# Performance work log

Measured on AMD Instinct MI355X. Metric: run time of the kernel, lower is better.

## Reference

```python
import jax, jax.numpy as jnp
import numpy as np

B, S, D = 32, 8192, 256  # batch, src_len, dim (context features = 2*D)


def setup_inputs() -> dict:
    key = jax.random.key(0)
    k0, k1, k2, k3, k4, k5 = jax.random.split(key, 6)
    inp = jax.random.normal(k0, (B, 1, D), jnp.float32)
    context = jax.random.normal(k1, (B, S, 2 * D), jnp.float32)
    Wa = jax.random.normal(k2, (D, D), jnp.float32) / np.sqrt(D)      # torch Linear weight [out,in]
    Ua = jax.random.normal(k3, (D, 2 * D), jnp.float32) / np.sqrt(2 * D)
    va = jax.random.normal(k4, (1, D), jnp.float32) / np.sqrt(D)
    context_lengths = jax.random.randint(k5, (B,), S // 2, S + 1).astype(jnp.int32)
    return {"input": inp, "context": context, "Wa": Wa, "Ua": Ua,
            "va": va, "context_lengths": context_lengths}


def reference(input, context, Wa, Ua, va, context_lengths):
    # score: va(Wa(h_t) + Ua(h_s)) -- additive (Bahdanau) attention, no nonlinearity
    q = jnp.einsum('btd,ed->bte', input, Wa)            # [B,1,D]
    k = jnp.einsum('bsc,ec->bse', context, Ua)          # [B,S,D]
    align = jnp.einsum('bsd,d->bs', q + k, va[0])       # [B,S] (targetL=1, squeezed)
    # mask positions >= context_lengths with -inf (sequence_mask + masked_fill_)
    mask = jnp.arange(S, dtype=jnp.int32)[None, :] < context_lengths[:, None]
    align = jnp.where(mask, align, -jnp.inf)
    attn = jax.nn.softmax(align, axis=-1)               # [B,S]
    c = jnp.einsum('bs,bsc->bc', attn, context)         # [B,2D]  (bmm)
    # 3D input with targetL=1 -> non-one-step branch: transpose(0,1)
    attn_h = c[None]                                    # [1,B,2D]
    align_vectors = attn[None]                          # [1,B,S]
    return attn_h, align_vectors
```

## Files before the change

### kernel.cpp

```cpp
#include <hip/hip_runtime.h>
#include <math.h>

#define Bn 32
#define Sn 8192
#define Dn 256
#define Cn 512
#define NBLK 1024
#define NEG_BIG (-1e30f)

#define WS_U     0
#define WS_QV    512
#define WS_PM    544
#define WS_PL    (WS_PM + NBLK)
#define WS_PLAN  (WS_PL + NBLK)
#define WS_ALIGN (WS_PLAN + NBLK)
#define WS_PACC  (WS_ALIGN + Bn * Sn)

__device__ inline void ga_partition(const int* __restrict__ lens, int k,
                                    int& b, int& t0, int& t1) {
  int TOT = 0;
#pragma unroll
  for (int i = 0; i < Bn; ++i) TOT += (lens[i] + 15) >> 4;
  int P = 0, bb = 0, offb = 0, cntb = 1, ntb = 1;
#pragma unroll
  for (int i = 0; i < Bn; ++i) {
    const int nt = (lens[i] + 15) >> 4;
    const int o0 = (P * NBLK) / TOT;
    const int o1 = ((P + nt) * NBLK) / TOT;
    if (k >= o0 && k < o1) { bb = i; offb = o0; cntb = o1 - o0; ntb = nt; }
    P += nt;
  }
  const int j = k - offb;
  b = bb;
  t0 = (j * ntb) / cntb;
  t1 = ((j + 1) * ntb) / cntb;
}

__device__ inline void ga_batch_range(const int* __restrict__ lens, int b,
                                      int& offb, int& cntb) {
  int TOT = 0;
#pragma unroll
  for (int i = 0; i < Bn; ++i) TOT += (lens[i] + 15) >> 4;
  int P = 0;
  for (int i = 0; i < b; ++i) P += (lens[i] + 15) >> 4;
  const int nt = (lens[b] + 15) >> 4;
  offb = (P * NBLK) / TOT;
  cntb = ((P + nt) * NBLK) / TOT - offb;
}

__global__ __launch_bounds__(256) void ga_prep(const float* __restrict__ input,
                                               const float* __restrict__ Wa,
                                               const float* __restrict__ Ua,
                                               const float* __restrict__ va,
                                               const int* __restrict__ lens,
                                               float* __restrict__ ws) {
  const int tid = threadIdx.x, bx = blockIdx.x;
  if (bx < 8) {
    const int c = bx * 64 + (tid & 63);
    const int q = tid >> 6;
    float acc = 0.f;
#pragma unroll 8
    for (int i = 0; i < 64; ++i) {
      const int d = q * 64 + i;
      acc += va[d] * Ua[(size_t)d * Cn + c];
    }
    __shared__ float sh[4][64];
    sh[q][tid & 63] = acc;
    __syncthreads();
    if (tid < 64)
      ws[WS_U + bx * 64 + tid] = sh[0][tid] + sh[1][tid] + sh[2][tid] + sh[3][tid];
  } else if (bx == 8) {
    __shared__ float wsh[Dn];
    float acc = 0.f;
#pragma unroll 8
    for (int e = 0; e < Dn; ++e)
      acc += va[e] * Wa[(size_t)e * Dn + tid];
    wsh[tid] = acc;
    __syncthreads();
    const int b = tid >> 3, l8 = tid & 7;
    float p = 0.f;
#pragma unroll
    for (int j = 0; j < Dn / 8; ++j) {
      const int d = l8 + j * 8;
      p += input[b * Dn + d] * wsh[d];
    }
    p += __shfl_xor(p, 1);
    p += __shfl_xor(p, 2);
    p += __shfl_xor(p, 4);
    if (l8 == 0) ws[WS_QV + b] = p;
  } else {
    const int k = (bx - 9) * 256 + tid;
    int b, t0, t1;
    ga_partition(lens, k, b, t0, t1);
    ((int*)ws)[WS_PLAN + k] = b | (t0 << 5) | (t1 << 17);
  }
}

__global__ __launch_bounds__(256, 4) void ga_main(const float* __restrict__ context,
                                                  const int* __restrict__ lens,
                                                  float* __restrict__ ws) {
  const int k = blockIdx.x;
  const int plan = ((const int*)ws)[WS_PLAN + k];
  const int b  = plan & 31;
  const int t0 = (plan >> 5)  & 0xFFF;
  const int t1 = (plan >> 17) & 0xFFF;
  const int tid  = threadIdx.x;
  const int wave = tid >> 6;
  const int lane = tid & 63;
  const int l16  = lane & 15;
  const int slot = lane >> 4;
  const int len = lens[b];
  const float qv = ws[WS_QV + b];

  const float4* uv = (const float4*)(ws + WS_U);
  float4 u0 = uv[l16 +  0], u1 = uv[l16 + 16], u2 = uv[l16 + 32], u3 = uv[l16 + 48];
  float4 u4 = uv[l16 + 64], u5 = uv[l16 + 80], u6 = uv[l16 + 96], u7 = uv[l16 + 112];

  float m = NEG_BIG, l = 0.f;
  float4 a0 = make_float4(0.f,0.f,0.f,0.f), a1 = a0, a2 = a0, a3 = a0;
  float4 a4 = a0, a5 = a0, a6 = a0, a7 = a0;

  const float* cbase = context + (size_t)b * Sn * Cn;
  float* alout = ws + WS_ALIGN + (size_t)b * Sn;

  for (int t = t0; t < t1; ++t) {
    const int s = t * 16 + wave * 4 + slot;
    const float4* p = (const float4*)(cbase + (size_t)s * Cn) + l16;
    const float4 f0 = p[0],  f1 = p[16], f2 = p[32], f3 = p[48];
    const float4 f4 = p[64], f5 = p[80], f6 = p[96], f7 = p[112];

    float dot = f0.x*u0.x + f0.y*u0.y + f0.z*u0.z + f0.w*u0.w
              + f1.x*u1.x + f1.y*u1.y + f1.z*u1.z + f1.w*u1.w
              + f2.x*u2.x + f2.y*u2.y + f2.z*u2.z + f2.w*u2.w
              + f3.x*u3.x + f3.y*u3.y + f3.z*u3.z + f3.w*u3.w
              + f4.x*u4.x + f4.y*u4.y + f4.z*u4.z + f4.w*u4.w
              + f5.x*u5.x + f5.y*u5.y + f5.z*u5.z + f5.w*u5.w
              + f6.x*u6.x + f6.y*u6.y + f6.z*u6.z + f6.w*u6.w
              + f7.x*u7.x + f7.y*u7.y + f7.z*u7.z + f7.w*u7.w;
    dot += __shfl_xor(dot, 1);
    dot += __shfl_xor(dot, 2);
    dot += __shfl_xor(dot, 4);
    dot += __shfl_xor(dot, 8);

    const bool valid = (s < len);
    const float al = valid ? (qv + dot) : -INFINITY;
    if (l16 == 0 && valid) alout[s] = al;

    const float mn = fmaxf(m, al);
    const float sc = __expf(m - mn);
    const float pw = __expf(al - mn);
    l = l * sc + pw;
    a0.x=a0.x*sc+pw*f0.x; a0.y=a0.y*sc+pw*f0.y; a0.z=a0.z*sc+pw*f0.z; a0.w=a0.w*sc+pw*f0.w;
    a1.x=a1.x*sc+pw*f1.x; a1.y=a1.y*sc+pw*f1.y; a1.z=a1.z*sc+pw*f1.z; a1.w=a1.w*sc+pw*f1.w;
    a2.x=a2.x*sc+pw*f2.x; a2.y=a2.y*sc+pw*f2.y; a2.z=a2.z*sc+pw*f2.z; a2.w=a2.w*sc+pw*f2.w;
    a3.x=a3.x*sc+pw*f3.x; a3.y=a3.y*sc+pw*f3.y; a3.z=a3.z*sc+pw*f3.z; a3.w=a3.w*sc+pw*f3.w;
    a4.x=a4.x*sc+pw*f4.x; a4.y=a4.y*sc+pw*f4.y; a4.z=a4.z*sc+pw*f4.z; a4.w=a4.w*sc+pw*f4.w;
    a5.x=a5.x*sc+pw*f5.x; a5.y=a5.y*sc+pw*f5.y; a5.z=a5.z*sc+pw*f5.z; a5.w=a5.w*sc+pw*f5.w;
    a6.x=a6.x*sc+pw*f6.x; a6.y=a6.y*sc+pw*f6.y; a6.z=a6.z*sc+pw*f6.z; a6.w=a6.w*sc+pw*f6.w;
    a7.x=a7.x*sc+pw*f7.x; a7.y=a7.y*sc+pw*f7.y; a7.z=a7.z*sc+pw*f7.z; a7.w=a7.w*sc+pw*f7.w;
    m = mn;
  }

  float mw = fmaxf(m, __shfl_xor(m, 16));
  mw = fmaxf(mw, __shfl_xor(mw, 32));
  const float fS = __expf(m - mw);
  float lw = l * fS;
  lw += __shfl_xor(lw, 16);
  lw += __shfl_xor(lw, 32);
#define MRG(A) \
  A.x*=fS; A.y*=fS; A.z*=fS; A.w*=fS; \
  A.x+=__shfl_xor(A.x,16); A.y+=__shfl_xor(A.y,16); A.z+=__shfl_xor(A.z,16); A.w+=__shfl_xor(A.w,16); \
  A.x+=__shfl_xor(A.x,32); A.y+=__shfl_xor(A.y,32); A.z+=__shfl_xor(A.z,32); A.w+=__shfl_xor(A.w,32);
  MRG(a0) MRG(a1) MRG(a2) MRG(a3) MRG(a4) MRG(a5) MRG(a6) MRG(a7)
#undef MRG

  __shared__ float msh[4], lsh[4];
  __shared__ float accsh[4][Cn];
  if (lane == 0) { msh[wave] = mw; lsh[wave] = lw; }
  if (slot == 0) {
    float4* arow = (float4*)accsh[wave];
    arow[l16 +  0] = a0;  arow[l16 + 16] = a1;
    arow[l16 + 32] = a2;  arow[l16 + 48] = a3;
    arow[l16 + 64] = a4;  arow[l16 + 80] = a5;
    arow[l16 + 96] = a6;  arow[l16 +112] = a7;
  }
  __syncthreads();

  const float M = fmaxf(fmaxf(msh[0], msh[1]), fmaxf(msh[2], msh[3]));
  const float e0 = __expf(msh[0] - M), e1 = __expf(msh[1] - M);
  const float e2 = __expf(msh[2] - M), e3 = __expf(msh[3] - M);
  float* pacc = ws + WS_PACC + (size_t)k * Cn;
  for (int ch = tid; ch < Cn; ch += 256)
    pacc[ch] = e0 * accsh[0][ch] + e1 * accsh[1][ch]
             + e2 * accsh[2][ch] + e3 * accsh[3][ch];
  if (tid == 0) {
    ws[WS_PM + k] = M;
    ws[WS_PL + k] = e0 * lsh[0] + e1 * lsh[1] + e2 * lsh[2] + e3 * lsh[3];
  }
}

__global__ __launch_bounds__(256) void ga_finalize(const float* __restrict__ ws,
                                                   const int* __restrict__ lens,
                                                   float* __restrict__ out) {
  const int b = blockIdx.x >> 3, p = blockIdx.x & 7;
  const int tid = threadIdx.x;
  int offb, cntb;
  ga_batch_range(lens, b, offb, cntb);

  __shared__ float wgt[128];
  __shared__ float red[4][64];
  __shared__ float Msh, Lish;

  if (tid < 64) {
    const float m0 = (tid      < cntb) ? ws[WS_PM + offb + tid]      : NEG_BIG;
    const float m1 = (tid + 64 < cntb) ? ws[WS_PM + offb + tid + 64] : NEG_BIG;
    float mm = fmaxf(m0, m1);
#pragma unroll
    for (int off = 32; off; off >>= 1) mm = fmaxf(mm, __shfl_xor(mm, off));
    const float w0 = __expf(m0 - mm);
    const float w1 = __expf(m1 - mm);
    wgt[tid] = w0;  wgt[tid + 64] = w1;
    float li = 0.f;
    if (tid      < cntb) li += ws[WS_PL + offb + tid]      * w0;
    if (tid + 64 < cntb) li += ws[WS_PL + offb + tid + 64] * w1;
#pragma unroll
    for (int off = 32; off; off >>= 1) li += __shfl_xor(li, off);
    if (tid == 0) { Msh = mm; Lish = 1.f / li; }
  }
  __syncthreads();
  const float M = Msh, Li = Lish;

  {
    const int c = p * 64 + (tid & 63), g = tid >> 6;
    const float* pacc = ws + WS_PACC + (size_t)offb * Cn;
    float s = 0.f;
    for (int i = g; i < cntb; i += 4) s += wgt[i] * pacc[(size_t)i * Cn + c];
    red[g][tid & 63] = s;
    __syncthreads();
    if (tid < 64)
      out[b * Cn + p * 64 + tid] =
          (red[0][tid] + red[1][tid] + red[2][tid] + red[3][tid]) * Li;
  }

  {
    const int len = lens[b];
    const float* al = ws + WS_ALIGN + (size_t)b * Sn;
    float* ao = out + Bn * Cn + (size_t)b * Sn;
    const int s0 = p * 1024 + tid * 4;
    const float4 v = *(const float4*)(al + s0);
    float4 o;
    o.x = (s0 + 0 < len) ? __expf(v.x - M) * Li : 0.f;
    o.y = (s0 + 1 < len) ? __expf(v.y - M) * Li : 0.f;
    o.z = (s0 + 2 < len) ? __expf(v.z - M) * Li : 0.f;
    o.w = (s0 + 3 < len) ? __expf(v.w - M) * Li : 0.f;
    *(float4*)(ao + s0) = o;
  }
}

extern "C" void kernel_launch(void* const* d_in, const int* in_sizes, int n_in,
                              void* d_out, int out_size, void* d_ws, size_t ws_size,
                              hipStream_t stream) {
  const float* input   = (const float*)d_in[0];
  const float* context = (const float*)d_in[1];
  const float* Wa      = (const float*)d_in[2];
  const float* Ua      = (const float*)d_in[3];
  const float* va      = (const float*)d_in[4];
  const int*   lens    = (const int*)d_in[5];
  float* out = (float*)d_out;
  float* ws  = (float*)d_ws;

  ga_prep<<<13, 256, 0, stream>>>(input, Wa, Ua, va, lens, ws);
  ga_main<<<NBLK, 256, 0, stream>>>(context, lens, ws);
  ga_finalize<<<Bn * 8, 256, 0, stream>>>(ws, lens, out);
}
```

Before: 102.7 us.

## Double-buffer context loads, shrink block count, and restructure prep/finalize reductions

The main loop is rewritten to prefetch the next 16-row tile of context into a second register set while the current tile is processed, aiming to hide global-memory latency. The block count drops from 1024 to 768 and the occupancy hint from 4 to 3 blocks per CU, making room for the extra registers. The u-vector prep now uses float4 loads with a 16-way reduction. Finalize now runs on 32 blocks per batch and reduces with wave shuffles instead of shared memory. The risks are register pressure from the doubled buffers and finalize assuming at most 64 partitions per batch.

```diff
diff --git a/kernel.cpp b/kernel.cpp
--- a/kernel.cpp
+++ b/kernel.cpp
@@ -5,7 +5,7 @@
 #define Sn 8192
 #define Dn 256
 #define Cn 512
-#define NBLK 1024
+#define NBLK 768
 #define NEG_BIG (-1e30f)
 
 #define WS_U     0
@@ -56,19 +56,27 @@
                                                float* __restrict__ ws) {
   const int tid = threadIdx.x, bx = blockIdx.x;
   if (bx < 8) {
-    const int c = bx * 64 + (tid & 63);
-    const int q = tid >> 6;
-    float acc = 0.f;
-#pragma unroll 8
-    for (int i = 0; i < 64; ++i) {
-      const int d = q * 64 + i;
-      acc += va[d] * Ua[(size_t)d * Cn + c];
-    }
-    __shared__ float sh[4][64];
-    sh[q][tid & 63] = acc;
+    const float4* Ua4 = (const float4*)Ua;
+    const int rg = tid >> 4, q = tid & 15;
+    float4 acc = make_float4(0.f, 0.f, 0.f, 0.f);
+#pragma unroll 4
+    for (int d = rg; d < Dn; d += 16) {
+      const float vd = va[d];
+      const float4 t = Ua4[(size_t)d * 128 + bx * 16 + q];
+      acc.x += vd * t.x; acc.y += vd * t.y; acc.z += vd * t.z; acc.w += vd * t.w;
+    }
+    __shared__ float4 sh4[16][16];
+    sh4[rg][q] = acc;
     __syncthreads();
-    if (tid < 64)
-      ws[WS_U + bx * 64 + tid] = sh[0][tid] + sh[1][tid] + sh[2][tid] + sh[3][tid];
+    if (tid < 16) {
+      float4 s = sh4[0][tid];
+#pragma unroll
+      for (int r = 1; r < 16; ++r) {
+        s.x += sh4[r][tid].x; s.y += sh4[r][tid].y;
+        s.z += sh4[r][tid].z; s.w += sh4[r][tid].w;
+      }
+      ((float4*)(ws + WS_U))[bx * 16 + tid] = s;
+    }
   } else if (bx == 8) {
     __shared__ float wsh[Dn];
     float acc = 0.f;
@@ -96,7 +104,46 @@
   }
 }
 
-__global__ __launch_bounds__(256, 4) void ga_main(const float* __restrict__ context,
+#define LOADT(F0,F1,F2,F3,F4,F5,F6,F7, T) do {                       \
+    const int s_ = (T) * 16 + wave * 4 + slot;                       \
+    const float4* p_ = (const float4*)(cbase + (size_t)s_ * Cn) + l16;\
+    F0 = p_[0];  F1 = p_[16]; F2 = p_[32]; F3 = p_[48];              \
+    F4 = p_[64]; F5 = p_[80]; F6 = p_[96]; F7 = p_[112];             \
+  } while (0)
+
+#define PROC(F0,F1,F2,F3,F4,F5,F6,F7, T) do {                        \
+    const int s_ = (T) * 16 + wave * 4 + slot;                       \
+    float dot = F0.x*u0.x + F0.y*u0.y + F0.z*u0.z + F0.w*u0.w        \
+              + F1.x*u1.x + F1.y*u1.y + F1.z*u1.z + F1.w*u1.w        \
+              + F2.x*u2.x + F2.y*u2.y + F2.z*u2.z + F2.w*u2.w        \
+              + F3.x*u3.x + F3.y*u3.y + F3.z*u3.z + F3.w*u3.w        \
+              + F4.x*u4.x + F4.y*u4.y + F4.z*u4.z + F4.w*u4.w        \
+              + F5.x*u5.x + F5.y*u5.y + F5.z*u5.z + F5.w*u5.w        \
+              + F6.x*u6.x + F6.y*u6.y + F6.z*u6.z + F6.w*u6.w        \
+              + F7.x*u7.x + F7.y*u7.y + F7.z*u7.z + F7.w*u7.w;       \
+    dot += __shfl_xor(dot, 1);                                       \
+    dot += __shfl_xor(dot, 2);                                       \
+    dot += __shfl_xor(dot, 4);                                       \
+    dot += __shfl_xor(dot, 8);                                       \
+    const bool valid = (s_ < len);                                   \
+    const float al = valid ? (qv + dot) : -INFINITY;                 \
+    if (l16 == 0 && valid) alout[s_] = al;                           \
+    const float mn = fmaxf(m, al);                                   \
+    const float sc = __expf(m - mn);                                 \
+    const float pw = __expf(al - mn);                                \
+    l = l * sc + pw;                                                 \
+    a0.x=a0.x*sc+pw*F0.x; a0.y=a0.y*sc+pw*F0.y; a0.z=a0.z*sc+pw*F0.z; a0.w=a0.w*sc+pw*F0.w; \
+    a1.x=a1.x*sc+pw*F1.x; a1.y=a1.y*sc+pw*F1.y; a1.z=a1.z*sc+pw*F1.z; a1.w=a1.w*sc+pw*F1.w; \
+    a2.x=a2.x*sc+pw*F2.x; a2.y=a2.y*sc+pw*F2.y; a2.z=a2.z*sc+pw*F2.z; a2.w=a2.w*sc+pw*F2.w; \
+    a3.x=a3.x*sc+pw*F3.x; a3.y=a3.y*sc+pw*F3.y; a3.z=a3.z*sc+pw*F3.z; a3.w=a3.w*sc+pw*F3.w; \
+    a4.x=a4.x*sc+pw*F4.x; a4.y=a4.y*sc+pw*F4.y; a4.z=a4.z*sc+pw*F4.z; a4.w=a4.w*sc+pw*F4.w; \
+    a5.x=a5.x*sc+pw*F5.x; a5.y=a5.y*sc+pw*F5.y; a5.z=a5.z*sc+pw*F5.z; a5.w=a5.w*sc+pw*F5.w; \
+    a6.x=a6.x*sc+pw*F6.x; a6.y=a6.y*sc+pw*F6.y; a6.z=a6.z*sc+pw*F6.z; a6.w=a6.w*sc+pw*F6.w; \
+    a7.x=a7.x*sc+pw*F7.x; a7.y=a7.y*sc+pw*F7.y; a7.z=a7.z*sc+pw*F7.z; a7.w=a7.w*sc+pw*F7.w; \
+    m = mn;                                                          \
+  } while (0)
+
+__global__ __launch_bounds__(256, 3) void ga_main(const float* __restrict__ context,
                                                   const int* __restrict__ lens,
                                                   float* __restrict__ ws) {
   const int k = blockIdx.x;
@@ -123,43 +170,21 @@
   const float* cbase = context + (size_t)b * Sn * Cn;
   float* alout = ws + WS_ALIGN + (size_t)b * Sn;
 
-  for (int t = t0; t < t1; ++t) {
-    const int s = t * 16 + wave * 4 + slot;
-    const float4* p = (const float4*)(cbase + (size_t)s * Cn) + l16;
-    const float4 f0 = p[0],  f1 = p[16], f2 = p[32], f3 = p[48];
-    const float4 f4 = p[64], f5 = p[80], f6 = p[96], f7 = p[112];
-
-    float dot = f0.x*u0.x + f0.y*u0.y + f0.z*u0.z + f0.w*u0.w
-              + f1.x*u1.x + f1.y*u1.y + f1.z*u1.z + f1.w*u1.w
-              + f2.x*u2.x + f2.y*u2.y + f2.z*u2.z + f2.w*u2.w
-              + f3.x*u3.x + f3.y*u3.y + f3.z*u3.z + f3.w*u3.w
-              + f4.x*u4.x + f4.y*u4.y + f4.z*u4.z + f4.w*u4.w
-              + f5.x*u5.x + f5.y*u5.y + f5.z*u5.z + f5.w*u5.w
-              + f6.x*u6.x + f6.y*u6.y + f6.z*u6.z + f6.w*u6.w
-              + f7.x*u7.x + f7.y*u7.y + f7.z*u7.z + f7.w*u7.w;
-    dot += __shfl_xor(dot, 1);
-    dot += __shfl_xor(dot, 2);
-    dot += __shfl_xor(dot, 4);
-    dot += __shfl_xor(dot, 8);
-
-    const bool valid = (s < len);
-    const float al = valid ? (qv + dot) : -INFINITY;
-    if (l16 == 0 && valid) alout[s] = al;
-
-    const float mn = fmaxf(m, al);
-    const float sc = __expf(m - mn);
-    const float pw = __expf(al - mn);
-    l = l * sc + pw;
-    a0.x=a0.x*sc+pw*f0.x; a0.y=a0.y*sc+pw*f0.y; a0.z=a0.z*sc+pw*f0.z; a0.w=a0.w*sc+pw*f0.w;
-    a1.x=a1.x*sc+pw*f1.x; a1.y=a1.y*sc+pw*f1.y; a1.z=a1.z*sc+pw*f1.z; a1.w=a1.w*sc+pw*f1.w;
-    a2.x=a2.x*sc+pw*f2.x; a2.y=a2.y*sc+pw*f2.y; a2.z=a2.z*sc+pw*f2.z; a2.w=a2.w*sc+pw*f2.w;
-    a3.x=a3.x*sc+pw*f3.x; a3.y=a3.y*sc+pw*f3.y; a3.z=a3.z*sc+pw*f3.z; a3.w=a3.w*sc+pw*f3.w;
-    a4.x=a4.x*sc+pw*f4.x; a4.y=a4.y*sc+pw*f4.y; a4.z=a4.z*sc+pw*f4.z; a4.w=a4.w*sc+pw*f4.w;
-    a5.x=a5.x*sc+pw*f5.x; a5.y=a5.y*sc+pw*f5.y; a5.z=a5.z*sc+pw*f5.z; a5.w=a5.w*sc+pw*f5.w;
-    a6.x=a6.x*sc+pw*f6.x; a6.y=a6.y*sc+pw*f6.y; a6.z=a6.z*sc+pw*f6.z; a6.w=a6.w*sc+pw*f6.w;
-    a7.x=a7.x*sc+pw*f7.x; a7.y=a7.y*sc+pw*f7.y; a7.z=a7.z*sc+pw*f7.z; a7.w=a7.w*sc+pw*f7.w;
-    m = mn;
-  }
+  float4 fa0, fa1, fa2, fa3, fa4, fa5, fa6, fa7;
+  float4 fb0, fb1, fb2, fb3, fb4, fb5, fb6, fb7;
+
+  int t = t0;
+  LOADT(fa0,fa1,fa2,fa3,fa4,fa5,fa6,fa7, t0);
+  while (t + 1 < t1) {
+    LOADT(fb0,fb1,fb2,fb3,fb4,fb5,fb6,fb7, t + 1);
+    PROC (fa0,fa1,fa2,fa3,fa4,fa5,fa6,fa7, t);
+    if (t + 2 < t1)
+      LOADT(fa0,fa1,fa2,fa3,fa4,fa5,fa6,fa7, t + 2);
+    PROC (fb0,fb1,fb2,fb3,fb4,fb5,fb6,fb7, t + 1);
+    t += 2;
+  }
+  if (t < t1)
+    PROC (fa0,fa1,fa2,fa3,fa4,fa5,fa6,fa7, t);
 
   float mw = fmaxf(m, __shfl_xor(m, 16));
   mw = fmaxf(mw, __shfl_xor(mw, 32));
@@ -202,58 +227,46 @@
 __global__ __launch_bounds__(256) void ga_finalize(const float* __restrict__ ws,
                                                    const int* __restrict__ lens,
                                                    float* __restrict__ out) {
-  const int b = blockIdx.x >> 3, p = blockIdx.x & 7;
+  const int b = blockIdx.x >> 5, p = blockIdx.x & 31;
   const int tid = threadIdx.x;
+  const int wave = tid >> 6, lane = tid & 63;
   int offb, cntb;
   ga_batch_range(lens, b, offb, cntb);
 
-  __shared__ float wgt[128];
-  __shared__ float red[4][64];
-  __shared__ float Msh, Lish;
-
-  if (tid < 64) {
-    const float m0 = (tid      < cntb) ? ws[WS_PM + offb + tid]      : NEG_BIG;
-    const float m1 = (tid + 64 < cntb) ? ws[WS_PM + offb + tid + 64] : NEG_BIG;
-    float mm = fmaxf(m0, m1);
-#pragma unroll
-    for (int off = 32; off; off >>= 1) mm = fmaxf(mm, __shfl_xor(mm, off));
-    const float w0 = __expf(m0 - mm);
-    const float w1 = __expf(m1 - mm);
-    wgt[tid] = w0;  wgt[tid + 64] = w1;
-    float li = 0.f;
-    if (tid      < cntb) li += ws[WS_PL + offb + tid]      * w0;
-    if (tid + 64 < cntb) li += ws[WS_PL + offb + tid + 64] * w1;
-#pragma unroll
-    for (int off = 32; off; off >>= 1) li += __shfl_xor(li, off);
-    if (tid == 0) { Msh = mm; Lish = 1.f / li; }
-  }
-  __syncthreads();
-  const float M = Msh, Li = Lish;
+  const float mi = (lane < cntb) ? ws[WS_PM + offb + lane] : NEG_BIG;
+  float mm = mi;
+#pragma unroll
+  for (int off = 32; off; off >>= 1) mm = fmaxf(mm, __shfl_xor(mm, off));
+  const float wgt = __expf(mi - mm);
+  float li = (lane < cntb) ? ws[WS_PL + offb + lane] * wgt : 0.f;
+#pragma unroll
+  for (int off = 32; off; off >>= 1) li += __shfl_xor(li, off);
+  const float Li = 1.f / li;
 
   {
-    const int c = p * 64 + (tid & 63), g = tid >> 6;
+    const int cc = lane >> 4, ii = lane & 15;
+    const int c = p * 16 + wave * 4 + cc;
     const float* pacc = ws + WS_PACC + (size_t)offb * Cn;
     float s = 0.f;
-    for (int i = g; i < cntb; i += 4) s += wgt[i] * pacc[(size_t)i * Cn + c];
-    red[g][tid & 63] = s;
-    __syncthreads();
-    if (tid < 64)
-      out[b * Cn + p * 64 + tid] =
-          (red[0][tid] + red[1][tid] + red[2][tid] + red[3][tid]) * Li;
+#pragma unroll
+    for (int kk = 0; kk < 4; ++kk) {
+      const int i = ii + 16 * kk;
+      const float w = __shfl(wgt, i);
+      if (i < cntb) s += w * pacc[(size_t)i * Cn + c];
+    }
+    s += __shfl_xor(s, 1);
+    s += __shfl_xor(s, 2);
+    s += __shfl_xor(s, 4);
+    s += __shfl_xor(s, 8);
+    if (ii == 0) out[b * Cn + c] = s * Li;
   }
 
   {
     const int len = lens[b];
+    const int s0 = p * 256 + tid;
     const float* al = ws + WS_ALIGN + (size_t)b * Sn;
-    float* ao = out + Bn * Cn + (size_t)b * Sn;
-    const int s0 = p * 1024 + tid * 4;
-    const float4 v = *(const float4*)(al + s0);
-    float4 o;
-    o.x = (s0 + 0 < len) ? __expf(v.x - M) * Li : 0.f;
-    o.y = (s0 + 1 < len) ? __expf(v.y - M) * Li : 0.f;
-    o.z = (s0 + 2 < len) ? __expf(v.z - M) * Li : 0.f;
-    o.w = (s0 + 3 < len) ? __expf(v.w - M) * Li : 0.f;
-    *(float4*)(ao + s0) = o;
+    out[Bn * Cn + (size_t)b * Sn + s0] =
+        (s0 < len) ? __expf(al[s0] - mm) * Li : 0.f;
   }
 }
 
@@ -269,7 +282,7 @@
   float* out = (float*)d_out;
   float* ws  = (float*)d_ws;
 
-  ga_prep<<<13, 256, 0, stream>>>(input, Wa, Ua, va, lens, ws);
+  ga_prep<<<12, 256, 0, stream>>>(input, Wa, Ua, va, lens, ws);
   ga_main<<<NBLK, 256, 0, stream>>>(context, lens, ws);
-  ga_finalize<<<Bn * 8, 256, 0, stream>>>(ws, lens, out);
-}
+  ga_finalize<<<Bn * 32, 256, 0, stream>>>(ws, lens, out);
+}
```

After: 125.3 us. 22.0% more time.
